# Kernel tuning notes

Measured on AMD Instinct MI355X. Metric: run time of the kernel, lower is better.

## Reference

```python
import jax, jax.numpy as jnp
import numpy as np

CONV_UNITS = 512   # conv (compressed) memory slots
SHORT_UNITS = 512  # short-term memory slots
RATE = 4           # compression rate == timesteps (required for fixed-size memory)


def setup_inputs() -> dict:
    key = jax.random.key(0)
    k1, k2, k3, k4 = jax.random.split(key, 4)
    B, T, F = 128, RATE, 1024
    inputs = jax.random.normal(k1, (B, T, F), dtype=jnp.float32)
    memory = jax.random.normal(k2, (CONV_UNITS + SHORT_UNITS, F), dtype=jnp.float32)
    kernel = jax.random.normal(k3, (RATE, F, F), dtype=jnp.float32) * 0.02  # (width, in_F, out_F)
    bias = jax.random.normal(k4, (F,), dtype=jnp.float32) * 0.02
    return {"inputs": inputs, "memory": memory, "kernel": kernel, "bias": bias}


def reference(inputs, memory, kernel, bias):
    """Compressive-transformer memory shift (method='conv', use_bias=True).

    inputs: (B, T, F); memory: (CONV_UNITS+SHORT_UNITS, F)
    Sequential over batch: each sample compresses the oldest T short-memory
    slots into one conv-memory slot (strided conv1d, SAME padding -> 1 step
    since T == RATE), shifts conv memory left by 1, and shifts the new sample
    into short memory. Returns memory snapshot after each sample: (B, M, F).
    """
    T = inputs.shape[1]

    def step(mem, x):  # mem: (M, F), x: (T, F)
        conv_mem = mem[:CONV_UNITS]
        short_mem = mem[CONV_UNITS:]
        old = short_mem[:T]  # oldest T short-memory slots, (T, F)
        # TF nn.conv1d(old[None], kernel, stride=RATE, padding='SAME');
        # with input length T == RATE and kernel width RATE, SAME adds no
        # padding and the output has exactly one step: (1, 1, F).
        comp = jax.lax.conv_general_dilated(
            old[None], kernel, window_strides=(RATE,), padding='SAME',
            dimension_numbers=('NWC', 'WIO', 'NWC'))[0] + bias  # (1, F)
        conv_new = jnp.concatenate([conv_mem[1:], comp], axis=0)      # shift-in compressed slot
        short_new = jnp.concatenate([short_mem[T:], x], axis=0)       # shift-in new sample
        new_mem = jnp.concatenate([conv_new, short_new], axis=0)      # (M, F)
        return new_mem, new_mem

    _, mems = jax.lax.scan(step, memory, inputs)  # (B, M, F)
    return mems
```

## Files before the change

kernel.cpp:

```cpp
#include <hip/hip_runtime.h>
#include <cstddef>

#define F       1024
#define NB      128
#define KK      4096
#define KSPLIT  8
#define KCHUNK  512
#define KT      32
#define BT      16
#define OT      256

typedef float f4 __attribute__((ext_vector_type(4)));
typedef float f2 __attribute__((ext_vector_type(2)));

__global__ __launch_bounds__(256) void gemm_partial(
    const float* __restrict__ mem, const float* __restrict__ kern,
    float* __restrict__ partial)
{
  const int ot = blockIdx.x, bt = blockIdx.y, ks = blockIdx.z;
  const int t  = threadIdx.x;
  const int tx = t & 63;
  const int ty = t >> 6;
  __shared__ float At[KT][BT];
  __shared__ float Bt[KT][OT];

  f4 acc[4] = {{0,0,0,0},{0,0,0,0},{0,0,0,0},{0,0,0,0}};
  const float* Ab = mem + 512 * F;

  for (int kc = 0; kc < KCHUNK; kc += KT) {
    const int k0 = ks * KCHUNK + kc;
    {
      const int b_l = t >> 4;
      const int k_l = (t & 15) * 2;
      f2 v = *(const f2*)(Ab + (size_t)(bt * BT + b_l) * KK + k0 + k_l);
      At[k_l][b_l]     = v.x;
      At[k_l + 1][b_l] = v.y;
    }
#pragma unroll
    for (int i = 0; i < 8; ++i) {
      const int fid = t + i * 256;
      const int r = fid >> 6, c4 = fid & 63;
      *(f4*)&Bt[r][c4 * 4] =
          *(const f4*)(kern + (size_t)(k0 + r) * F + ot * OT + c4 * 4);
    }
    __syncthreads();
#pragma unroll
    for (int k = 0; k < KT; ++k) {
      f4 a  = *(const f4*)&At[k][ty * 4];
      f4 bv = *(const f4*)&Bt[k][tx * 4];
      acc[0] += a.x * bv;
      acc[1] += a.y * bv;
      acc[2] += a.z * bv;
      acc[3] += a.w * bv;
    }
    __syncthreads();
  }
  float* p = partial + ((size_t)ks * NB + bt * BT + ty * 4) * F + ot * OT + tx * 4;
#pragma unroll
  for (int i = 0; i < 4; ++i) *(f4*)(p + (size_t)i * F) = acc[i];
}

__global__ __launch_bounds__(256) void reduce_comp(
    const float* __restrict__ partial, const float* __restrict__ bias,
    float* __restrict__ comp)
{
  const int idx = blockIdx.x * 256 + threadIdx.x;
  float s = bias[idx & (F - 1)];
#pragma unroll
  for (int ks = 0; ks < KSPLIT; ++ks) s += partial[(size_t)ks * NB * F + idx];
  comp[idx] = s;
}

__global__ __launch_bounds__(256) void writer(
    const float* __restrict__ inputs, const float* __restrict__ mem,
    const float* __restrict__ comp, float* __restrict__ out)
{
  const int t = threadIdx.x;
  const int base = blockIdx.x * 4;
#pragma unroll
  for (int r = 0; r < 4; ++r) {
    const int gid = base + r;
    const int b = gid >> 10, row = gid & 1023;
    const float* src;
    if (row < 512) {
      const int lim1 = 511 - b;
      src = (row < lim1) ? (mem + (size_t)(b + 1 + row) * F)
                         : (comp + (size_t)(row - lim1) * F);
    } else {
      const int r2 = row - 512;
      const int c2 = 508 - 4 * b;
      src = (r2 < c2) ? (mem + (size_t)(516 + 4 * b + r2) * F)
                      : (inputs + (size_t)(r2 - c2) * F);
    }
    const f4 v = *(const f4*)(src + t * 4);
    __builtin_nontemporal_store(v, (f4*)(out + (size_t)gid * F + t * 4));
  }
}

extern "C" void kernel_launch(void* const* d_in, const int* in_sizes, int n_in,
                              void* d_out, int out_size, void* d_ws, size_t ws_size,
                              hipStream_t stream) {
  const float* inputs = (const float*)d_in[0];
  const float* memory = (const float*)d_in[1];
  const float* kern   = (const float*)d_in[2];
  const float* bias   = (const float*)d_in[3];
  float* out = (float*)d_out;

  float* partial = (float*)d_ws;
  float* comp    = partial + (size_t)KSPLIT * NB * F;

  gemm_partial<<<dim3(4, 8, 8), 256, 0, stream>>>(memory, kern, partial);
  reduce_comp<<<dim3(512), 256, 0, stream>>>(partial, bias, comp);
  writer<<<dim3(32768), 256, 0, stream>>>(inputs, memory, comp, out);
}
```

Baseline: 571.4 us.

## Fuse GEMM with bulk memory copy and scatter compressed slots directly

Merges the split-K GEMM and the bulk memory-copy writer into one launch, interleaving GEMM blocks among the writer blocks so compute overlaps the output copy. The writer skips the compressed-slot rows, and a second kernel reduces the split-K partials plus bias and writes each compressed slot straight into every output snapshot that needs it. This removes one launch, the intermediate comp buffer and the serialization between GEMM and copy. In exchange the scatter kernel does scattered row writes after the main copy, and the GEMM blocks compete with copy blocks for CU resources.

After: 615.2 us. +7.7%, slower.

```diff
diff --git a/kernel.cpp b/kernel.cpp
--- a/kernel.cpp
+++ b/kernel.cpp
@@ -9,74 +9,66 @@
 #define KT      32
 #define BT      16
 #define OT      256
+#define NGEMM   256
+#define NWRITE  32768
 
 typedef float f4 __attribute__((ext_vector_type(4)));
 typedef float f2 __attribute__((ext_vector_type(2)));
 
-__global__ __launch_bounds__(256) void gemm_partial(
-    const float* __restrict__ mem, const float* __restrict__ kern,
-    float* __restrict__ partial)
+__global__ __launch_bounds__(256) void fused_bulk(
+    const float* __restrict__ inputs, const float* __restrict__ mem,
+    const float* __restrict__ kern, float* __restrict__ partial,
+    float* __restrict__ out)
 {
-  const int ot = blockIdx.x, bt = blockIdx.y, ks = blockIdx.z;
-  const int t  = threadIdx.x;
-  const int tx = t & 63;
-  const int ty = t >> 6;
   __shared__ float At[KT][BT];
   __shared__ float Bt[KT][OT];
+  const int bid = blockIdx.x;
+  const int t   = threadIdx.x;
 
-  f4 acc[4] = {{0,0,0,0},{0,0,0,0},{0,0,0,0},{0,0,0,0}};
-  const float* Ab = mem + 512 * F;
+  if (bid < 4 * NGEMM && (bid & 3) == 0) {
+    const int g  = bid >> 2;
+    const int ot = g & 3, bt = (g >> 2) & 7, ks = g >> 5;
+    const int tx = t & 63;
+    const int ty = t >> 6;
+    f4 acc[4] = {{0,0,0,0},{0,0,0,0},{0,0,0,0},{0,0,0,0}};
+    const float* Ab = mem + 512 * F;
 
-  for (int kc = 0; kc < KCHUNK; kc += KT) {
-    const int k0 = ks * KCHUNK + kc;
-    {
-      const int b_l = t >> 4;
-      const int k_l = (t & 15) * 2;
-      f2 v = *(const f2*)(Ab + (size_t)(bt * BT + b_l) * KK + k0 + k_l);
-      At[k_l][b_l]     = v.x;
-      At[k_l + 1][b_l] = v.y;
+    for (int kc = 0; kc < KCHUNK; kc += KT) {
+      const int k0 = ks * KCHUNK + kc;
+      {
+        const int b_l = t >> 4;
+        const int k_l = (t & 15) * 2;
+        f2 v = *(const f2*)(Ab + (size_t)(bt * BT + b_l) * KK + k0 + k_l);
+        At[k_l][b_l]     = v.x;
+        At[k_l + 1][b_l] = v.y;
+      }
+#pragma unroll
+      for (int i = 0; i < 8; ++i) {
+        const int fid = t + i * 256;
+        const int r = fid >> 6, c4 = fid & 63;
+        *(f4*)&Bt[r][c4 * 4] =
+            *(const f4*)(kern + (size_t)(k0 + r) * F + ot * OT + c4 * 4);
+      }
+      __syncthreads();
+#pragma unroll
+      for (int k = 0; k < KT; ++k) {
+        f4 a  = *(const f4*)&At[k][ty * 4];
+        f4 bv = *(const f4*)&Bt[k][tx * 4];
+        acc[0] += a.x * bv;
+        acc[1] += a.y * bv;
+        acc[2] += a.z * bv;
+        acc[3] += a.w * bv;
+      }
+      __syncthreads();
     }
+    float* p = partial + ((size_t)ks * NB + bt * BT + ty * 4) * F + ot * OT + tx * 4;
 #pragma unroll
-    for (int i = 0; i < 8; ++i) {
-      const int fid = t + i * 256;
-      const int r = fid >> 6, c4 = fid & 63;
-      *(f4*)&Bt[r][c4 * 4] =
-          *(const f4*)(kern + (size_t)(k0 + r) * F + ot * OT + c4 * 4);
-    }
-    __syncthreads();
-#pragma unroll
-    for (int k = 0; k < KT; ++k) {
-      f4 a  = *(const f4*)&At[k][ty * 4];
-      f4 bv = *(const f4*)&Bt[k][tx * 4];
-      acc[0] += a.x * bv;
-      acc[1] += a.y * bv;
-      acc[2] += a.z * bv;
-      acc[3] += a.w * bv;
-    }
-    __syncthreads();
+    for (int i = 0; i < 4; ++i) *(f4*)(p + (size_t)i * F) = acc[i];
+    return;
   }
-  float* p = partial + ((size_t)ks * NB + bt * BT + ty * 4) * F + ot * OT + tx * 4;
-#pragma unroll
-  for (int i = 0; i < 4; ++i) *(f4*)(p + (size_t)i * F) = acc[i];
-}
 
-__global__ __launch_bounds__(256) void reduce_comp(
-    const float* __restrict__ partial, const float* __restrict__ bias,
-    float* __restrict__ comp)
-{
-  const int idx = blockIdx.x * 256 + threadIdx.x;
-  float s = bias[idx & (F - 1)];
-#pragma unroll
-  for (int ks = 0; ks < KSPLIT; ++ks) s += partial[(size_t)ks * NB * F + idx];
-  comp[idx] = s;
-}
-
-__global__ __launch_bounds__(256) void writer(
-    const float* __restrict__ inputs, const float* __restrict__ mem,
-    const float* __restrict__ comp, float* __restrict__ out)
-{
-  const int t = threadIdx.x;
-  const int base = blockIdx.x * 4;
+  const int w    = (bid < 4 * NGEMM) ? (bid - (bid >> 2) - 1) : (bid - NGEMM);
+  const int base = w * 4;
 #pragma unroll
   for (int r = 0; r < 4; ++r) {
     const int gid = base + r;
@@ -84,8 +76,8 @@
     const float* src;
     if (row < 512) {
       const int lim1 = 511 - b;
-      src = (row < lim1) ? (mem + (size_t)(b + 1 + row) * F)
-                         : (comp + (size_t)(row - lim1) * F);
+      if (row >= lim1) continue;
+      src = mem + (size_t)(b + 1 + row) * F;
     } else {
       const int r2 = row - 512;
       const int c2 = 508 - 4 * b;
@@ -94,6 +86,30 @@
     }
     const f4 v = *(const f4*)(src + t * 4);
     __builtin_nontemporal_store(v, (f4*)(out + (size_t)gid * F + t * 4));
+  }
+}
+
+__global__ __launch_bounds__(256) void comp_scatter(
+    const float* __restrict__ partial, const float* __restrict__ bias,
+    float* __restrict__ out)
+{
+  const int bid = blockIdx.x;
+  const int c  = bid >> 3;
+  const int jb = bid & 7;
+  const int b0 = jb * 16;
+  if (b0 + 15 < c) return;
+
+  const int t = threadIdx.x;
+  f4 s = *(const f4*)(bias + t * 4);
+#pragma unroll
+  for (int ks = 0; ks < KSPLIT; ++ks)
+    s += *(const f4*)(partial + ((size_t)ks * NB + c) * F + t * 4);
+
+  const int blo = (b0 > c) ? b0 : c;
+  const int bhi = (b0 + 15 < 127) ? (b0 + 15) : 127;
+  for (int b = blo; b <= bhi; ++b) {
+    float* dst = out + ((size_t)b * 1024 + (511 - b + c)) * F + t * 4;
+    __builtin_nontemporal_store(s, (f4*)dst);
   }
 }
 
@@ -107,9 +123,8 @@
   float* out = (float*)d_out;
 
   float* partial = (float*)d_ws;
-  float* comp    = partial + (size_t)KSPLIT * NB * F;
 
-  gemm_partial<<<dim3(4, 8, 8), 256, 0, stream>>>(memory, kern, partial);
-  reduce_comp<<<dim3(512), 256, 0, stream>>>(partial, bias, comp);
-  writer<<<dim3(32768), 256, 0, stream>>>(inputs, memory, comp, out);
+  fused_bulk<<<dim3(NWRITE + NGEMM), 256, 0, stream>>>(inputs, memory, kern,
+                                                       partial, out);
+  comp_scatter<<<dim3(1024), 256, 0, stream>>>(partial, bias, out);
 }
```
